# Kernel tuning notes

Hardware: AMD Instinct MI355X
Metric: run time of the kernel (lower is better)

Reference implementation:

```python
import jax, jax.numpy as jnp
import numpy as np

ANCHORS = jnp.array([1.3221, 1.73145, 3.19275, 4.00944, 5.05587,
                     8.09892, 9.47112, 4.84053, 11.2364, 10.0071], dtype=jnp.float32)
GRID, NA, NC, CH = 13, 5, 20, 25  # grid size, anchors, classes, channels per anchor


def setup_inputs() -> dict:
    key = jax.random.key(0)
    k1, k2, k3 = jax.random.split(key, 3)
    B, O = 2048, 32
    det = jax.random.normal(k1, (B, NA * CH, GRID, GRID), dtype=jnp.float32)
    gt_boxes = jax.random.uniform(k2, (B, O, 4), dtype=jnp.float32)  # x,y,w,h in [0,1)
    gt_class = jax.random.randint(k3, (B, O), 0, NC)
    return {"detection_result": det, "gt_boxes": gt_boxes, "gt_class": gt_class}


def _forward(det, gt_boxes, gt_class):
    B, O = gt_boxes.shape[0], gt_boxes.shape[1]
    d = det.reshape(B, NA, CH, GRID, GRID)
    # scale predicted w,h by anchor priors / grid (the in-place loop in torch)
    wh = ANCHORS.reshape(NA, 2) / GRID
    scale = jnp.ones((NA, CH), det.dtype).at[:, 2:4].set(wh)
    d = d * scale[None, :, :, None, None]

    N = B * O
    gb = gt_boxes.reshape(N, 4)
    x, y, w, h = gb[:, 0], gb[:, 1], gb[:, 2], gb[:, 3]
    cls = gt_class.reshape(N)
    b_idx = jnp.repeat(jnp.arange(B), O)
    gx = jnp.floor(x * GRID).astype(jnp.int32)
    gy = jnp.floor(y * GRID).astype(jnp.int32)

    # gather the 5 anchor-box predictions at each object's cell: [N, 5, 4]
    pred = d[b_idx, :, :4, gy, gx]
    px, py, pw, ph = pred[..., 0], pred[..., 1], pred[..., 2], pred[..., 3]
    bx0 = (px + gx[:, None]) / GRID - pw / 2
    by0 = (py + gy[:, None]) / GRID - ph / 2
    bx1, by1 = bx0 + pw, by0 + ph
    gx0, gy0 = (x - w / 2)[:, None], (y - h / 2)[:, None]
    gx1, gy1 = (x + w / 2)[:, None], (y + h / 2)[:, None]
    ix0 = jnp.maximum(gx0, bx0); iy0 = jnp.maximum(gy0, by0)
    ix1 = jnp.minimum(gx1, bx1); iy1 = jnp.minimum(gy1, by1)
    inter = (ix1 - ix0 + 1) * (iy1 - iy0 + 1)  # faithful +1 from source
    a1 = (gx1 - gx0 + 1) * (gy1 - gy0 + 1)
    a2 = (bx1 - bx0 + 1) * (by1 - by0 + 1)
    iou = inter / (a1 + a2 - inter)
    aidx = jnp.argmax(iou, axis=1).astype(jnp.int32)  # best anchor per object

    tx, ty = x * GRID - gx, y * GRID - gy
    onehot = jax.nn.one_hot(cls, NC, dtype=det.dtype)
    vals = jnp.concatenate(
        [jnp.stack([tx, ty, w, h, jnp.ones_like(x)], axis=1), onehot], axis=1)  # [N,25]
    wvals = jnp.concatenate(
        [jnp.array([5., 5., 5., 5., 1.]), jnp.ones(NC)]).astype(det.dtype)

    # sequential torch writes deterministically
    S = B * NA * GRID * GRID
    flat = ((b_idx * NA + aidx) * GRID + gy) * GRID + gx
    owner = jnp.full((S,), -1, jnp.int32).at[flat].max(jnp.arange(N, dtype=jnp.int32))
    valid = owner >= 0
    gt_slot = jnp.where(valid[:, None], vals[jnp.clip(owner, 0)], 0.0)  # [S,25]
    w_slot = jnp.where(valid[:, None], wvals[None, :], 0.0)
    gt_grid = gt_slot.reshape(B, NA, GRID, GRID, CH).transpose(0, 1, 4, 2, 3)
    weight = w_slot.reshape(B, NA, GRID, GRID, CH).transpose(0, 1, 4, 2, 3)

    obj = gt_grid[:, :, 4] == 1.0  # [B,5,13,13]
    weight = weight.at[:, :, 4].set(jnp.where(obj, weight[:, :, 4], 0.5))

    wse = weight * (gt_grid - d) ** 2
    loss = jnp.sum(wse)
    obj_f = obj.astype(det.dtype)
    obj_loss = jnp.sum(obj_f[:, :, None] * wse[:, :, 0:5])
    no_obj_loss = jnp.sum((1.0 - obj_f) * wse[:, :, 4])
    conf_loss = jnp.sum(obj_f[:, :, None] * wse[:, :, 5:25])
    return loss, obj_loss, no_obj_loss, conf_loss


def reference(detection_result, gt_boxes, gt_class):
    return _forward(detection_result, gt_boxes, gt_class)
```

## Files before the change

kernel.cpp:

```cpp
#include <hip/hip_runtime.h>

#define GRIDSZ 13
#define NANCH  5
#define NCHAN  25
#define BATCH  2048
#define NOBJ   32
#define PLANE  (GRIDSZ * GRIDSZ)

__constant__ float AW[NANCH] = {1.3221f / 13.0f, 3.19275f / 13.0f, 5.05587f / 13.0f,
                                9.47112f / 13.0f, 11.2364f / 13.0f};
__constant__ float AH[NANCH] = {1.73145f / 13.0f, 4.00944f / 13.0f, 8.09892f / 13.0f,
                                4.84053f / 13.0f, 10.0071f / 13.0f};

__global__ void __launch_bounds__(256) main_kernel(const float* __restrict__ det,
                                                   const float* __restrict__ gt_boxes,
                                                   const int* __restrict__ gt_class,
                                                   float4* __restrict__ partials) {
    int b = blockIdx.x;
    int t = threadIdx.x;
    __shared__ float  iou_sm[NOBJ * NANCH];
    __shared__ float4 pred_sm[NOBJ * NANCH];
    __shared__ float4 box_sm[NOBJ];
    __shared__ int    gx_sm[NOBJ], gy_sm[NOBJ];
    __shared__ int    cls_sm[NOBJ];
    __shared__ int    flat_sm[NOBJ];
    __shared__ int    aidx_sm[NOBJ];
    __shared__ int    win_sm[NOBJ];
    __shared__ float  sm4[4][4];

    const float* detb = det + (size_t)b * (NANCH * NCHAN) * PLANE;

    float loss = 0.0f, objl = 0.0f, noobjl = 0.0f, confl = 0.0f;

    if (t < NOBJ * NANCH) {
        int gt = t / NANCH, a = t - gt * NANCH;
        float4 g = ((const float4*)gt_boxes)[b * NOBJ + gt];
        float x = g.x, y = g.y, w = g.z, h = g.w;
        int gx = (int)floorf(x * 13.0f);
        int gy = (int)floorf(y * 13.0f);
        if (a == 0) {
            gx_sm[gt] = gx; gy_sm[gt] = gy;
            box_sm[gt] = g;
            cls_sm[gt] = gt_class[b * NOBJ + gt];
        }
        const float* p = detb + (size_t)a * NCHAN * PLANE + gy * GRIDSZ + gx;
        float px = p[0];
        float py = p[PLANE];
        float pw = p[2 * PLANE] * AW[a];
        float ph = p[3 * PLANE] * AH[a];
        float gx0 = x - w * 0.5f, gy0 = y - h * 0.5f;
        float gx1 = x + w * 0.5f, gy1 = y + h * 0.5f;
        float a1 = (gx1 - gx0 + 1.0f) * (gy1 - gy0 + 1.0f);
        float bx0 = (px + (float)gx) / 13.0f - pw * 0.5f;
        float by0 = (py + (float)gy) / 13.0f - ph * 0.5f;
        float bx1 = bx0 + pw, by1 = by0 + ph;
        float ix0 = fmaxf(gx0, bx0), iy0 = fmaxf(gy0, by0);
        float ix1 = fminf(gx1, bx1), iy1 = fminf(gy1, by1);
        float inter = (ix1 - ix0 + 1.0f) * (iy1 - iy0 + 1.0f);
        float a2 = (bx1 - bx0 + 1.0f) * (by1 - by0 + 1.0f);
        iou_sm[t] = inter / (a1 + a2 - inter);
        pred_sm[t] = make_float4(px, py, pw, ph);
    }

    {
        float s = 0.0f;
        for (int idx = t; idx < NANCH * PLANE; idx += 256) {
            int a = idx / PLANE, i = idx - a * PLANE;
            float d = detb[((size_t)a * NCHAN + 4) * PLANE + i];
            s += d * d;
        }
        loss += 0.5f * s;
        noobjl += 0.5f * s;
    }

    __syncthreads();

    if (t < NOBJ) {
        float best = -INFINITY;
        int aidx = 0;
        #pragma unroll
        for (int a = 0; a < NANCH; ++a) {
            float v = iou_sm[t * NANCH + a];
            if (v > best) { best = v; aidx = a; }
        }
        aidx_sm[t] = aidx;
        flat_sm[t] = (aidx * GRIDSZ + gy_sm[t]) * GRIDSZ + gx_sm[t];
    }
    __syncthreads();

    if (t < NOBJ) {
        int f = flat_sm[t];
        int winner = 1;
        for (int m = t + 1; m < NOBJ; ++m)
            if (flat_sm[m] == f) winner = 0;
        win_sm[t] = winner;
    }
    __syncthreads();

    if (t < NOBJ && win_sm[t]) {
        int aidx = aidx_sm[t];
        float4 pr = pred_sm[t * NANCH + aidx];
        float4 g = box_sm[t];
        int gx = gx_sm[t], gy = gy_sm[t];
        const float* p = detb + (size_t)aidx * NCHAN * PLANE + gy * GRIDSZ + gx;
        float d4 = p[4 * PLANE];
        float tx = g.x * 13.0f - (float)gx;
        float ty = g.y * 13.0f - (float)gy;
        float e, tt, corr = 0.0f;
        e = tx - pr.x;  tt = 5.0f * e * e; corr += tt; objl += tt;
        e = ty - pr.y;  tt = 5.0f * e * e; corr += tt; objl += tt;
        e = g.z - pr.z; tt = 5.0f * e * e; corr += tt; objl += tt;
        e = g.w - pr.w; tt = 5.0f * e * e; corr += tt; objl += tt;
        e = 1.0f - d4;  tt = e * e;        corr += tt; objl += tt;
        float sub = 0.5f * d4 * d4;
        loss += corr - sub;
        noobjl -= sub;
    }

    for (int item = t; item < NOBJ * 20; item += 256) {
        int gt = item / 20;
        int c = 5 + (item - gt * 20);
        if (win_sm[gt]) {
            int aidx = aidx_sm[gt];
            float d = detb[((size_t)aidx * NCHAN + c) * PLANE + gy_sm[gt] * GRIDSZ + gx_sm[gt]];
            float gtv = (c - 5 == cls_sm[gt]) ? 1.0f : 0.0f;
            float e = gtv - d;
            float tt = e * e;
            loss += tt;
            confl += tt;
        }
    }

    #pragma unroll
    for (int off = 32; off > 0; off >>= 1) {
        loss   += __shfl_down(loss, off);
        objl   += __shfl_down(objl, off);
        noobjl += __shfl_down(noobjl, off);
        confl  += __shfl_down(confl, off);
    }
    int lane = t & 63;
    int wid  = t >> 6;
    if (lane == 0) {
        sm4[wid][0] = loss; sm4[wid][1] = objl; sm4[wid][2] = noobjl; sm4[wid][3] = confl;
    }
    __syncthreads();
    if (t == 0) {
        float s0 = 0, s1 = 0, s2 = 0, s3 = 0;
        #pragma unroll
        for (int i = 0; i < 4; ++i) {
            s0 += sm4[i][0]; s1 += sm4[i][1]; s2 += sm4[i][2]; s3 += sm4[i][3];
        }
        partials[blockIdx.x] = make_float4(s0, s1, s2, s3);
    }
}

__global__ void reduce_kernel(const float4* __restrict__ partials,
                              float* __restrict__ out) {
    float s0 = 0, s1 = 0, s2 = 0, s3 = 0;
    for (int i = threadIdx.x; i < BATCH; i += 256) {
        float4 v = partials[i];
        s0 += v.x; s1 += v.y; s2 += v.z; s3 += v.w;
    }
    #pragma unroll
    for (int off = 32; off > 0; off >>= 1) {
        s0 += __shfl_down(s0, off);
        s1 += __shfl_down(s1, off);
        s2 += __shfl_down(s2, off);
        s3 += __shfl_down(s3, off);
    }
    __shared__ float sm[4][4];
    int lane = threadIdx.x & 63;
    int wid  = threadIdx.x >> 6;
    if (lane == 0) {
        sm[wid][0] = s0; sm[wid][1] = s1; sm[wid][2] = s2; sm[wid][3] = s3;
    }
    __syncthreads();
    if (threadIdx.x == 0) {
        float a0 = 0, a1 = 0, a2 = 0, a3 = 0;
        #pragma unroll
        for (int i = 0; i < 4; ++i) {
            a0 += sm[i][0]; a1 += sm[i][1]; a2 += sm[i][2]; a3 += sm[i][3];
        }
        out[0] = a0; out[1] = a1; out[2] = a2; out[3] = a3;
    }
}

extern "C" void kernel_launch(void* const* d_in, const int* in_sizes, int n_in,
                              void* d_out, int out_size, void* d_ws, size_t ws_size,
                              hipStream_t stream) {
    const float* det = (const float*)d_in[0];
    const float* gtb = (const float*)d_in[1];
    const int*   gtc = (const int*)d_in[2];
    float* out = (float*)d_out;
    float4* partials = (float4*)d_ws;

    main_kernel<<<BATCH, 256, 0, stream>>>(det, gtb, gtc, partials);
    reduce_kernel<<<1, 256, 0, stream>>>(partials, out);
}
```

Baseline: 33.43 us.

## Map one batch element per wavefront and replace block barriers with wave shuffles

Each 64-lane wavefront now processes a single batch element, with four batch elements per 256-thread block. Block-wide __syncthreads and the cross-wave shared-memory reduction are removed. Shuffles handle box broadcast and winner detection, and each wave writes its own partial directly. This is meant to cut barrier and idle-thread overhead. The cost is that each wave loops serially over the 160 anchor/object IoU gathers, and correctness relies on implicit wave-synchronous shared-memory visibility.

```diff
diff --git a/kernel.cpp b/kernel.cpp
--- a/kernel.cpp
+++ b/kernel.cpp
@@ -5,7 +5,10 @@
 #define NCHAN  25
 #define BATCH  2048
 #define NOBJ   32
-#define PLANE  (GRIDSZ * GRIDSZ)
+#define PLANE  169
+#define ACH    (NCHAN * PLANE)
+#define WPB    4
+#define NBLK   (BATCH / WPB)
 
 __constant__ float AW[NANCH] = {1.3221f / 13.0f, 3.19275f / 13.0f, 5.05587f / 13.0f,
                                 9.47112f / 13.0f, 11.2364f / 13.0f};
@@ -16,34 +19,53 @@
                                                    const float* __restrict__ gt_boxes,
                                                    const int* __restrict__ gt_class,
                                                    float4* __restrict__ partials) {
-    int b = blockIdx.x;
-    int t = threadIdx.x;
-    __shared__ float  iou_sm[NOBJ * NANCH];
-    __shared__ float4 pred_sm[NOBJ * NANCH];
-    __shared__ float4 box_sm[NOBJ];
-    __shared__ int    gx_sm[NOBJ], gy_sm[NOBJ];
-    __shared__ int    cls_sm[NOBJ];
-    __shared__ int    flat_sm[NOBJ];
-    __shared__ int    aidx_sm[NOBJ];
-    __shared__ int    win_sm[NOBJ];
-    __shared__ float  sm4[4][4];
+    int wv   = threadIdx.x >> 6;
+    int lane = threadIdx.x & 63;
+    int batch = blockIdx.x * WPB + wv;
 
-    const float* detb = det + (size_t)b * (NANCH * NCHAN) * PLANE;
+    __shared__ float iou_sm[WPB][NOBJ * NANCH];
+    __shared__ int   gx_sm[WPB][NOBJ], gy_sm[WPB][NOBJ], cls_sm[WPB][NOBJ];
+    __shared__ int   aidx_sm[WPB][NOBJ], win_sm[WPB][NOBJ];
 
-    float loss = 0.0f, objl = 0.0f, noobjl = 0.0f, confl = 0.0f;
+    const float* detb = det + (size_t)batch * (NANCH * ACH);
 
-    if (t < NOBJ * NANCH) {
-        int gt = t / NANCH, a = t - gt * NANCH;
-        float4 g = ((const float4*)gt_boxes)[b * NOBJ + gt];
-        float x = g.x, y = g.y, w = g.z, h = g.w;
-        int gx = (int)floorf(x * 13.0f);
-        int gy = (int)floorf(y * 13.0f);
-        if (a == 0) {
-            gx_sm[gt] = gx; gy_sm[gt] = gy;
-            box_sm[gt] = g;
-            cls_sm[gt] = gt_class[b * NOBJ + gt];
+    float4 g = make_float4(0.f, 0.f, 0.f, 0.f);
+    int gx = 0, gy = 0;
+    if (lane < NOBJ) {
+        g = ((const float4*)gt_boxes)[batch * NOBJ + lane];
+        gx = (int)floorf(g.x * 13.0f);
+        gy = (int)floorf(g.y * 13.0f);
+        gx_sm[wv][lane]  = gx;
+        gy_sm[wv][lane]  = gy;
+        cls_sm[wv][lane] = gt_class[batch * NOBJ + lane];
+    }
+
+    float loss = 0.f, objl = 0.f, noobjl = 0.f, confl = 0.f;
+
+    {
+        float s = 0.f;
+        #pragma unroll
+        for (int a = 0; a < NANCH; ++a) {
+            const float* p = detb + (a * NCHAN + 4) * PLANE;
+            for (int pos = lane; pos < PLANE; pos += 64) {
+                float d = p[pos];
+                s += d * d;
+            }
         }
-        const float* p = detb + (size_t)a * NCHAN * PLANE + gy * GRIDSZ + gx;
+        loss   += 0.5f * s;
+        noobjl += 0.5f * s;
+    }
+
+    for (int pair = lane; pair < NOBJ * NANCH; pair += 64) {
+        int gt = pair / NANCH;
+        int a  = pair - gt * NANCH;
+        float x = __shfl(g.x, gt);
+        float y = __shfl(g.y, gt);
+        float w = __shfl(g.z, gt);
+        float h = __shfl(g.w, gt);
+        int gxv = gx_sm[wv][gt], gyv = gy_sm[wv][gt];
+        int pos = gyv * GRIDSZ + gxv;
+        const float* p = detb + (size_t)a * ACH + pos;
         float px = p[0];
         float py = p[PLANE];
         float pw = p[2 * PLANE] * AW[a];
@@ -51,83 +73,70 @@
         float gx0 = x - w * 0.5f, gy0 = y - h * 0.5f;
         float gx1 = x + w * 0.5f, gy1 = y + h * 0.5f;
         float a1 = (gx1 - gx0 + 1.0f) * (gy1 - gy0 + 1.0f);
-        float bx0 = (px + (float)gx) / 13.0f - pw * 0.5f;
-        float by0 = (py + (float)gy) / 13.0f - ph * 0.5f;
+        float bx0 = (px + (float)gxv) / 13.0f - pw * 0.5f;
+        float by0 = (py + (float)gyv) / 13.0f - ph * 0.5f;
         float bx1 = bx0 + pw, by1 = by0 + ph;
         float ix0 = fmaxf(gx0, bx0), iy0 = fmaxf(gy0, by0);
         float ix1 = fminf(gx1, bx1), iy1 = fminf(gy1, by1);
         float inter = (ix1 - ix0 + 1.0f) * (iy1 - iy0 + 1.0f);
         float a2 = (bx1 - bx0 + 1.0f) * (by1 - by0 + 1.0f);
-        iou_sm[t] = inter / (a1 + a2 - inter);
-        pred_sm[t] = make_float4(px, py, pw, ph);
+        iou_sm[wv][pair] = inter / (a1 + a2 - inter);
     }
 
-    {
-        float s = 0.0f;
-        for (int idx = t; idx < NANCH * PLANE; idx += 256) {
-            int a = idx / PLANE, i = idx - a * PLANE;
-            float d = detb[((size_t)a * NCHAN + 4) * PLANE + i];
-            s += d * d;
+    int aidx = 0, flat = -1, win = 0;
+    if (lane < NOBJ) {
+        float best = -INFINITY;
+        #pragma unroll
+        for (int a = 0; a < NANCH; ++a) {
+            float v = iou_sm[wv][lane * NANCH + a];
+            if (v > best) { best = v; aidx = a; }
         }
-        loss += 0.5f * s;
-        noobjl += 0.5f * s;
+        flat = (aidx * GRIDSZ + gy) * GRIDSZ + gx;
+        win = 1;
+    }
+    #pragma unroll
+    for (int m = 1; m < NOBJ; ++m) {
+        int fm = __shfl(flat, m);
+        if (lane < NOBJ && m > lane && fm == flat) win = 0;
+    }
+    if (lane < NOBJ) {
+        aidx_sm[wv][lane] = aidx;
+        win_sm[wv][lane]  = win;
     }
 
-    __syncthreads();
-
-    if (t < NOBJ) {
-        float best = -INFINITY;
-        int aidx = 0;
-        #pragma unroll
-        for (int a = 0; a < NANCH; ++a) {
-            float v = iou_sm[t * NANCH + a];
-            if (v > best) { best = v; aidx = a; }
-        }
-        aidx_sm[t] = aidx;
-        flat_sm[t] = (aidx * GRIDSZ + gy_sm[t]) * GRIDSZ + gx_sm[t];
-    }
-    __syncthreads();
-
-    if (t < NOBJ) {
-        int f = flat_sm[t];
-        int winner = 1;
-        for (int m = t + 1; m < NOBJ; ++m)
-            if (flat_sm[m] == f) winner = 0;
-        win_sm[t] = winner;
-    }
-    __syncthreads();
-
-    if (t < NOBJ && win_sm[t]) {
-        int aidx = aidx_sm[t];
-        float4 pr = pred_sm[t * NANCH + aidx];
-        float4 g = box_sm[t];
-        int gx = gx_sm[t], gy = gy_sm[t];
-        const float* p = detb + (size_t)aidx * NCHAN * PLANE + gy * GRIDSZ + gx;
+    if (lane < NOBJ && win) {
+        int pos = gy * GRIDSZ + gx;
+        const float* p = detb + (size_t)aidx * ACH + pos;
+        float px = p[0];
+        float py = p[PLANE];
+        float pw = p[2 * PLANE] * AW[aidx];
+        float ph = p[3 * PLANE] * AH[aidx];
         float d4 = p[4 * PLANE];
         float tx = g.x * 13.0f - (float)gx;
         float ty = g.y * 13.0f - (float)gy;
-        float e, tt, corr = 0.0f;
-        e = tx - pr.x;  tt = 5.0f * e * e; corr += tt; objl += tt;
-        e = ty - pr.y;  tt = 5.0f * e * e; corr += tt; objl += tt;
-        e = g.z - pr.z; tt = 5.0f * e * e; corr += tt; objl += tt;
-        e = g.w - pr.w; tt = 5.0f * e * e; corr += tt; objl += tt;
-        e = 1.0f - d4;  tt = e * e;        corr += tt; objl += tt;
+        float e, t, corr = 0.f;
+        e = tx - px;   t = 5.0f * e * e; corr += t; objl += t;
+        e = ty - py;   t = 5.0f * e * e; corr += t; objl += t;
+        e = g.z - pw;  t = 5.0f * e * e; corr += t; objl += t;
+        e = g.w - ph;  t = 5.0f * e * e; corr += t; objl += t;
+        e = 1.0f - d4; t = e * e;        corr += t; objl += t;
         float sub = 0.5f * d4 * d4;
-        loss += corr - sub;
+        loss   += corr - sub;
         noobjl -= sub;
     }
 
-    for (int item = t; item < NOBJ * 20; item += 256) {
+    for (int item = lane; item < NOBJ * 20; item += 64) {
         int gt = item / 20;
-        int c = 5 + (item - gt * 20);
-        if (win_sm[gt]) {
-            int aidx = aidx_sm[gt];
-            float d = detb[((size_t)aidx * NCHAN + c) * PLANE + gy_sm[gt] * GRIDSZ + gx_sm[gt]];
-            float gtv = (c - 5 == cls_sm[gt]) ? 1.0f : 0.0f;
+        int c  = 5 + (item - gt * 20);
+        if (win_sm[wv][gt]) {
+            int av = aidx_sm[wv][gt];
+            float d = detb[((size_t)av * NCHAN + c) * PLANE +
+                           gy_sm[wv][gt] * GRIDSZ + gx_sm[wv][gt]];
+            float gtv = (c - 5 == cls_sm[wv][gt]) ? 1.0f : 0.0f;
             float e = gtv - d;
-            float tt = e * e;
-            loss += tt;
-            confl += tt;
+            float t = e * e;
+            loss  += t;
+            confl += t;
         }
     }
 
@@ -138,19 +147,8 @@
         noobjl += __shfl_down(noobjl, off);
         confl  += __shfl_down(confl, off);
     }
-    int lane = t & 63;
-    int wid  = t >> 6;
     if (lane == 0) {
-        sm4[wid][0] = loss; sm4[wid][1] = objl; sm4[wid][2] = noobjl; sm4[wid][3] = confl;
-    }
-    __syncthreads();
-    if (t == 0) {
-        float s0 = 0, s1 = 0, s2 = 0, s3 = 0;
-        #pragma unroll
-        for (int i = 0; i < 4; ++i) {
-            s0 += sm4[i][0]; s1 += sm4[i][1]; s2 += sm4[i][2]; s3 += sm4[i][3];
-        }
-        partials[blockIdx.x] = make_float4(s0, s1, s2, s3);
+        partials[batch] = make_float4(loss, objl, noobjl, confl);
     }
 }
 
@@ -194,6 +192,6 @@
     float* out = (float*)d_out;
     float4* partials = (float4*)d_ws;
 
-    main_kernel<<<BATCH, 256, 0, stream>>>(det, gtb, gtc, partials);
+    main_kernel<<<NBLK, 256, 0, stream>>>(det, gtb, gtc, partials);
     reduce_kernel<<<1, 256, 0, stream>>>(partials, out);
 }
```

Result: slower. 37.77 us (+13.0%).
